# Kernel optimization log

Measured on AMD Instinct MI355X. Metric: run time of the kernel, lower is better.

## Reference

```python
import jax, jax.numpy as jnp
import numpy as np

B, M, D = 4, 2048, 1024


def setup_inputs() -> dict:
    key = jax.random.key(0)
    k1, k2, k3, k4 = jax.random.split(key, 4)
    x = jax.random.normal(k1, (B, M, D), dtype=jnp.float32)
    scale = 0.02
    wq = jax.random.normal(k2, (D, D), dtype=jnp.float32) * scale
    wk = jax.random.normal(k3, (D, D), dtype=jnp.float32) * scale
    wv = jax.random.normal(k4, (D, D), dtype=jnp.float32) * scale
    return {"x": x, "wq": wq, "wk": wk, "wv": wv}


def _rope_tables(m, d):
    # Faithful to source: phi = 10000 ** (-2*(i-1)/d)  (note the (i-1), incl. i=0)
    i = jnp.arange(d // 2, dtype=jnp.float32)
    phi = jnp.power(10000.0, -2.0 * (i - 1.0) / d)  # [d/2]
    pos = jnp.arange(m, dtype=jnp.float32)
    ang = pos[:, None] * phi[None, :]  # [m, d/2]
    return jnp.cos(ang), jnp.sin(ang)


def _apply_rope(t, cos, sin):
    # Original does t[pos] @ R[pos] (row-vector times rotation matrix):
    #   out_even =  t_even*cos + t_odd*sin
    #   out_odd  = -t_even*sin + t_odd*cos
    te = t[..., 0::2]  # [b, m, d/2]
    to = t[..., 1::2]
    oe = te * cos + to * sin
    oo = -te * sin + to * cos
    return jnp.stack([oe, oo], axis=-1).reshape(t.shape)


def reference(x, wq, wk, wv):
    b, m, d = x.shape
    q = x @ wq.T
    k = x @ wk.T
    v = x @ wv.T
    cos, sin = _rope_tables(m, d)
    qr = _apply_rope(q, cos, sin)
    kr = _apply_rope(k, cos, sin)
    # causal SDPA (dropout disabled for deterministic reference)
    scores = jnp.einsum('bqd,bkd->bqk', qr, kr) / jnp.sqrt(jnp.float32(d))
    causal = jnp.tril(jnp.ones((m, m), dtype=bool))
    scores = jnp.where(causal[None, :, :], scores, jnp.finfo(scores.dtype).min)
    attn = jax.nn.softmax(scores, axis=-1)
    return jnp.einsum('bqk,bkd->bqd', attn, v)
```

## Files before the change

### kernel.cpp

```cpp
#include <hip/hip_runtime.h>
#include <hip/hip_bf16.h>
#include <math.h>


typedef __bf16 bf16x8 __attribute__((ext_vector_type(8)));
typedef float  f32x4  __attribute__((ext_vector_type(4)));

__device__ __forceinline__ ushort f2bf(float f) {
    __hip_bfloat16 h = __float2bfloat16(f);
    return *reinterpret_cast<ushort*>(&h);
}

__device__ __forceinline__ void async_load16(const ushort* g, ushort* l) {
    __builtin_amdgcn_global_load_lds(
        (const __attribute__((address_space(1))) void*)g,
        (__attribute__((address_space(3))) void*)l, 16, 0, 0);
}

__global__ __launch_bounds__(256) void cvt_all_kernel(
    const float* __restrict__ x,  const float* __restrict__ wq,
    const float* __restrict__ wk, const float* __restrict__ wv,
    ushort* __restrict__ xb, ushort* __restrict__ wqb,
    ushort* __restrict__ wkb, ushort* __restrict__ wvb,
    float2* __restrict__ cs)
{
    const int t = blockIdx.y;
    if (t == 4) {
        const int idx = blockIdx.x * 256 + threadIdx.x;
        if (idx < 2048 * 512) {
            const int pos = idx >> 9, i = idx & 511;
            const float phi = powf(10000.0f, -2.0f * ((float)i - 1.0f) / 1024.0f);
            float s, c;
            sincosf((float)pos * phi, &s, &c);
            cs[idx] = make_float2(c, s);
        }
        return;
    }
    const float* in  = (t == 0) ? x  : (t == 1) ? wq  : (t == 2) ? wk  : wv;
    ushort*      out = (t == 0) ? xb : (t == 1) ? wqb : (t == 2) ? wkb : wvb;
    const int n4 = (t == 0) ? 2097152 : 262144;
    int i = blockIdx.x * blockDim.x + threadIdx.x;
    if (i < n4) {
        float4 f = ((const float4*)in)[i];
        ushort4 o;
        o.x = f2bf(f.x); o.y = f2bf(f.y); o.z = f2bf(f.z); o.w = f2bf(f.w);
        ((ushort4*)out)[i] = o;
    }
}

__device__ __forceinline__ void gemm128_core_sb(
    const ushort* __restrict__ A, const ushort* __restrict__ B,
    int lda, int ldb, int m0, int n0, int kIters,
    ushort* As, ushort* Bs, f32x4 acc[4][4])
{
    const int tid  = threadIdx.x;
    const int lane = tid & 63, wave = tid >> 6;
    const int wm = (wave >> 1) * 64, wn = (wave & 1) * 64;
    const int quad = lane >> 4, l16 = lane & 15;
    const int srow = lane >> 2, c = lane & 3;
    const int rr   = wave * 32 + srow;
    const int cc   = c ^ ((rr >> 1) & 3);
    const int scol = cc * 8;

    const ushort* ag0 = A + (size_t)(m0 + rr) * lda + scol;
    const ushort* bg0 = B + (size_t)(n0 + rr) * ldb + scol;
    const ushort* ag1 = ag0 + (size_t)16 * lda;
    const ushort* bg1 = bg0 + (size_t)16 * ldb;
    ushort* la0 = As + (wave * 32) * 32;
    ushort* la1 = la0 + 16 * 32;
    ushort* lb0 = Bs + (wave * 32) * 32;
    ushort* lb1 = lb0 + 16 * 32;

    for (int kt = 0; kt < kIters; ++kt) {
        const int k0 = kt * 32;
        async_load16(ag0 + k0, la0);
        async_load16(ag1 + k0, la1);
        async_load16(bg0 + k0, lb0);
        async_load16(bg1 + k0, lb1);
        __syncthreads();
        bf16x8 aF[4], bF[4];
#pragma unroll
        for (int i = 0; i < 4; ++i) {
            const int r = wm + i * 16 + l16;
            aF[i] = *(const bf16x8*)(As + r * 32 + ((quad ^ ((r >> 1) & 3)) * 8));
        }
#pragma unroll
        for (int j = 0; j < 4; ++j) {
            const int r = wn + j * 16 + l16;
            bF[j] = *(const bf16x8*)(Bs + r * 32 + ((quad ^ ((r >> 1) & 3)) * 8));
        }
#pragma unroll
        for (int i = 0; i < 4; ++i)
#pragma unroll
            for (int j = 0; j < 4; ++j)
                acc[i][j] = __builtin_amdgcn_mfma_f32_16x16x32_bf16(aF[i], bF[j], acc[i][j], 0, 0, 0);
        __syncthreads();
    }
}

__device__ __forceinline__ void gemm128_core_ring(
    const ushort* __restrict__ A, const ushort* __restrict__ B,
    int lda, int ldb, int m0, int n0, int kIters,
    ushort* L, f32x4 acc[4][4])
{
    const int tid  = threadIdx.x;
    const int lane = tid & 63, wave = tid >> 6;
    const int wm = (wave >> 1) * 64, wn = (wave & 1) * 64;
    const int quad = lane >> 4, l16 = lane & 15;
    const int srow = lane >> 2, c = lane & 3;
    const int rr   = wave * 32 + srow;
    const int cc   = c ^ ((rr >> 1) & 3);
    const int scol = cc * 8;

    const ushort* ag0 = A + (size_t)(m0 + rr) * lda + scol;
    const ushort* bg0 = B + (size_t)(n0 + rr) * ldb + scol;
    const ushort* ag1 = ag0 + (size_t)16 * lda;
    const ushort* bg1 = bg0 + (size_t)16 * ldb;
    const int lofs = (wave * 32) * 32;

#define RING_STAGE(KT, BUF) do {                                   \
        const int _k0 = (KT) * 32;                                 \
        ushort* _la = L + (BUF) * 4096 + lofs;                     \
        ushort* _lb = L + 12288 + (BUF) * 4096 + lofs;             \
        async_load16(ag0 + _k0, _la);                              \
        async_load16(ag1 + _k0, _la + 16 * 32);                    \
        async_load16(bg0 + _k0, _lb);                              \
        async_load16(bg1 + _k0, _lb + 16 * 32);                    \
    } while (0)

    RING_STAGE(0, 0);
    if (kIters > 1) RING_STAGE(1, 1);

    int buf = 0;
    for (int kt = 0; kt < kIters; ++kt) {
        if (kt + 1 < kIters) {
            asm volatile("s_waitcnt vmcnt(4)" ::: "memory");
        } else {
            asm volatile("s_waitcnt vmcnt(0)" ::: "memory");
        }
        __builtin_amdgcn_s_barrier();
        asm volatile("" ::: "memory");
        if (kt + 2 < kIters) {
            int nb = buf + 2; if (nb >= 3) nb -= 3;
            RING_STAGE(kt + 2, nb);
        }
        const ushort* as = L + buf * 4096;
        const ushort* bs = L + 12288 + buf * 4096;
        bf16x8 aF[4], bF[4];
#pragma unroll
        for (int i = 0; i < 4; ++i) {
            const int r = wm + i * 16 + l16;
            aF[i] = *(const bf16x8*)(as + r * 32 + ((quad ^ ((r >> 1) & 3)) * 8));
        }
#pragma unroll
        for (int j = 0; j < 4; ++j) {
            const int r = wn + j * 16 + l16;
            bF[j] = *(const bf16x8*)(bs + r * 32 + ((quad ^ ((r >> 1) & 3)) * 8));
        }
#pragma unroll
        for (int i = 0; i < 4; ++i)
#pragma unroll
            for (int j = 0; j < 4; ++j)
                acc[i][j] = __builtin_amdgcn_mfma_f32_16x16x32_bf16(aF[i], bF[j], acc[i][j], 0, 0, 0);
        buf += 1; if (buf == 3) buf = 0;
    }
#undef RING_STAGE
}

#define ACC_INIT4(acc) \
    _Pragma("unroll") for (int i = 0; i < 4; ++i) \
    _Pragma("unroll") for (int j = 0; j < 4; ++j) \
    _Pragma("unroll") for (int r = 0; r < 4; ++r) acc[i][j][r] = 0.0f;

__global__ __launch_bounds__(256) void qkv_rope_kernel(
    const ushort* __restrict__ xb, const ushort* __restrict__ wq,
    const ushort* __restrict__ wk, const ushort* __restrict__ wv,
    const float2* __restrict__ cs,
    ushort* __restrict__ Qr, ushort* __restrict__ Kr, ushort* __restrict__ VT)
{
    __shared__ __attribute__((aligned(16))) ushort As[128 * 32];
    __shared__ __attribute__((aligned(16))) ushort Bs[128 * 32];
    const int m0 = blockIdx.x * 128;
    const int n0 = blockIdx.y * 128;
    const int z  = blockIdx.z;
    const ushort* W = (z == 0) ? wq : (z == 1) ? wk : wv;

    f32x4 acc[4][4];
    ACC_INIT4(acc)
    gemm128_core_sb(xb, W, 1024, 1024, m0, n0, 32, As, Bs, acc);

    const int lane = threadIdx.x & 63, wave = threadIdx.x >> 6;
    const int wm = (wave >> 1) * 64, wn = (wave & 1) * 64;
    const int quad = lane >> 4, l16 = lane & 15;

    if (z < 2) {
        ushort* out = (z == 0) ? Qr : Kr;
#pragma unroll
        for (int j = 0; j < 4; ++j) {
            const int n = n0 + wn + j * 16 + l16;
            const int iidx = n >> 1;
            const bool odd = n & 1;
#pragma unroll
            for (int i = 0; i < 4; ++i) {
                const int mbase = m0 + wm + i * 16 + quad * 4;
                const int pos0  = mbase & 2047;
                const float2* csp = cs + (size_t)pos0 * 512 + iidx;
#pragma unroll
                for (int r = 0; r < 4; ++r) {
                    const float2 sc = csp[(size_t)r * 512];
                    float v = acc[i][j][r];
                    float p = __shfl_xor(v, 1);
                    float o = odd ? (v * sc.x - p * sc.y) : (v * sc.x + p * sc.y);
                    out[(size_t)(mbase + r) * 1024 + n] = f2bf(o);
                }
            }
        }
    } else {
#pragma unroll
        for (int i = 0; i < 4; ++i) {
            const int mbase = m0 + wm + i * 16 + quad * 4;
            const int b = mbase >> 11, pos0 = mbase & 2047;
#pragma unroll
            for (int j = 0; j < 4; ++j) {
                const int n = n0 + wn + j * 16 + l16;
                ushort4 o;
                o.x = f2bf(acc[i][j][0]); o.y = f2bf(acc[i][j][1]);
                o.z = f2bf(acc[i][j][2]); o.w = f2bf(acc[i][j][3]);
                *(ushort4*)(VT + ((size_t)b * 1024 + n) * 2048 + pos0) = o;
            }
        }
    }
}

__global__ __launch_bounds__(256) void scores_kernel(
    const ushort* __restrict__ Qr, const ushort* __restrict__ Kr,
    float* __restrict__ S)
{
    const int m0 = blockIdx.x * 128;
    const int n0 = blockIdx.y * 128;
    if (n0 > m0 + 127) return;
    const int b = blockIdx.z;
    __shared__ __attribute__((aligned(16))) ushort L[6 * 4096];
    const ushort* A = Qr + (size_t)b * 2048 * 1024;
    const ushort* B = Kr + (size_t)b * 2048 * 1024;
    float* Sb = S + (size_t)b * 2048 * 2048;

    f32x4 acc[4][4];
    ACC_INIT4(acc)
    gemm128_core_ring(A, B, 1024, 1024, m0, n0, 32, L, acc);

    const int lane = threadIdx.x & 63, wave = threadIdx.x >> 6;
    const int wm = (wave >> 1) * 64, wn = (wave & 1) * 64;
    const int quad = lane >> 4, l16 = lane & 15;
#pragma unroll
    for (int i = 0; i < 4; ++i)
#pragma unroll
        for (int j = 0; j < 4; ++j) {
            const int n = n0 + wn + j * 16 + l16;
#pragma unroll
            for (int r = 0; r < 4; ++r) {
                const int m = m0 + wm + i * 16 + quad * 4 + r;
                Sb[(size_t)m * 2048 + n] = acc[i][j][r] * 0.03125f;
            }
        }
}

__global__ __launch_bounds__(256) void softmax_kernel(
    const float* __restrict__ S, ushort* __restrict__ P)
{
    __shared__ float red[256];
    const int row = blockIdx.x, tid = threadIdx.x, b = blockIdx.y;
    const float* s = S + ((size_t)b * 2048 + row) * 2048;
    ushort*      p = P + ((size_t)b * 2048 + row) * 2048;
    const int nvalid = row + 1;
    const int wlimit = (row & ~127) + 128;
    const int j0 = tid * 8;

    float v[8] = {0.0f, 0.0f, 0.0f, 0.0f, 0.0f, 0.0f, 0.0f, 0.0f};
    if (j0 < nvalid) {
        float4 f0 = *(const float4*)(s + j0);
        v[0]=f0.x; v[1]=f0.y; v[2]=f0.z; v[3]=f0.w;
    }
    if (j0 + 4 < nvalid) {
        float4 f1 = *(const float4*)(s + j0 + 4);
        v[4]=f1.x; v[5]=f1.y; v[6]=f1.z; v[7]=f1.w;
    }

    float mx = -3.402823466e38f;
#pragma unroll
    for (int u = 0; u < 8; ++u) if (j0 + u < nvalid) mx = fmaxf(mx, v[u]);
    red[tid] = mx; __syncthreads();
    for (int off = 128; off > 0; off >>= 1) {
        if (tid < off) red[tid] = fmaxf(red[tid], red[tid + off]);
        __syncthreads();
    }
    mx = red[0]; __syncthreads();

    float sum = 0.0f;
#pragma unroll
    for (int u = 0; u < 8; ++u) {
        v[u] = (j0 + u < nvalid) ? __expf(v[u] - mx) : 0.0f;
        sum += v[u];
    }
    red[tid] = sum; __syncthreads();
    for (int off = 128; off > 0; off >>= 1) {
        if (tid < off) red[tid] += red[tid + off];
        __syncthreads();
    }
    const float inv = 1.0f / red[0];

    if (j0 < wlimit) {
        ushort o[8];
#pragma unroll
        for (int u = 0; u < 8; ++u) o[u] = f2bf(v[u] * inv);
        *(int4*)(p + j0) = *(const int4*)o;
    }
}

__global__ __launch_bounds__(256) void pv_kernel(
    const ushort* __restrict__ P, const ushort* __restrict__ VT,
    float* __restrict__ out)
{
    __shared__ __attribute__((aligned(16))) ushort L[6 * 4096];
    const int x  = blockIdx.x;
    const int mt = (x & 1) ? (15 - (x >> 1)) : (x >> 1);
    const int m0 = mt * 128;
    const int n0 = blockIdx.y * 128;
    const int b  = blockIdx.z;
    const ushort* A = P + (size_t)b * 2048 * 2048;
    const ushort* B = VT + (size_t)b * 1024 * 2048;
    const int kIters = (m0 + 128) / 32;

    f32x4 acc[4][4];
    ACC_INIT4(acc)
    gemm128_core_ring(A, B, 2048, 2048, m0, n0, kIters, L, acc);

    const int lane = threadIdx.x & 63, wave = threadIdx.x >> 6;
    const int wm = (wave >> 1) * 64, wn = (wave & 1) * 64;
    const int quad = lane >> 4, l16 = lane & 15;
#pragma unroll
    for (int i = 0; i < 4; ++i)
#pragma unroll
        for (int j = 0; j < 4; ++j) {
            const int n = n0 + wn + j * 16 + l16;
#pragma unroll
            for (int r = 0; r < 4; ++r) {
                const int m = m0 + wm + i * 16 + quad * 4 + r;
                out[((size_t)b * 2048 + m) * 1024 + n] = acc[i][j][r];
            }
        }
}

extern "C" void kernel_launch(void* const* d_in, const int* in_sizes, int n_in,
                              void* d_out, int out_size, void* d_ws, size_t ws_size,
                              hipStream_t stream) {
    const float* x  = (const float*)d_in[0];
    const float* wq = (const float*)d_in[1];
    const float* wk = (const float*)d_in[2];
    const float* wv = (const float*)d_in[3];

    const size_t MiB = 1024 * 1024;
    char* ws = (char*)d_ws;
    ushort* xb  = (ushort*)(ws);
    ushort* wqb = (ushort*)(ws +  16 * MiB);
    ushort* wkb = (ushort*)(ws +  18 * MiB);
    ushort* wvb = (ushort*)(ws +  20 * MiB);
    ushort* Qr  = (ushort*)(ws +  22 * MiB);
    ushort* Kr  = (ushort*)(ws +  38 * MiB);
    ushort* VT  = (ushort*)(ws +  54 * MiB);
    float*  S   = (float* )(ws +  70 * MiB);
    ushort* P   = (ushort*)(ws + 134 * MiB);
    float2* cs  = (float2*)(ws + 166 * MiB);
    float*  out = (float*)d_out;

    cvt_all_kernel <<<dim3(8192, 5),   256, 0, stream>>>(x, wq, wk, wv, xb, wqb, wkb, wvb, cs);
    qkv_rope_kernel<<<dim3(64, 8, 3),  256, 0, stream>>>(xb, wqb, wkb, wvb, cs, Qr, Kr, VT);
    scores_kernel  <<<dim3(16, 16, 4), 256, 0, stream>>>(Qr, Kr, S);
    softmax_kernel <<<dim3(2048, 4),   256, 0, stream>>>(S, P);
    pv_kernel      <<<dim3(16, 8, 4),  256, 0, stream>>>(P, VT, out);
}
```

Baseline: 271.6 us.

## Fuse softmax into scores epilogue and PV prologue via per-tile max/sum

Removes the standalone softmax kernel. The scores kernel now computes per-row max and exp-sum for each 128-column tile, and the PV kernel combines these tile stats, exponentiates the fp32 scores on the fly into bf16 shared-memory tiles, and rescales the output by the inverse row sum. This drops one launch and the write/read of the bf16 P matrix, but the PV kernel now reads fp32 scores (twice the bytes of P) and does exp work inside its main loop, with only double-buffered manual staging instead of the previous ring pipeline.

```diff
diff --git a/kernel.cpp b/kernel.cpp
--- a/kernel.cpp
+++ b/kernel.cpp
@@ -15,6 +15,19 @@
     __builtin_amdgcn_global_load_lds(
         (const __attribute__((address_space(1))) void*)g,
         (__attribute__((address_space(3))) void*)l, 16, 0, 0);
+}
+
+__device__ __forceinline__ void stage_a16(
+    ushort* dst, float4 lo, float4 hi, float m, int nv)
+{
+    float s[8] = {lo.x, lo.y, lo.z, lo.w, hi.x, hi.y, hi.z, hi.w};
+    ushort o[8];
+#pragma unroll
+    for (int u = 0; u < 8; ++u) {
+        const float e = (u < nv) ? __expf(s[u] - m) : 0.0f;
+        o[u] = f2bf(e);
+    }
+    *(int4*)dst = *(const int4*)o;
 }
 
 __global__ __launch_bounds__(256) void cvt_all_kernel(
@@ -234,13 +247,15 @@
 
 __global__ __launch_bounds__(256) void scores_kernel(
     const ushort* __restrict__ Qr, const ushort* __restrict__ Kr,
-    float* __restrict__ S)
+    float* __restrict__ S, float* __restrict__ Smax, float* __restrict__ Ssum)
 {
     const int m0 = blockIdx.x * 128;
     const int n0 = blockIdx.y * 128;
     if (n0 > m0 + 127) return;
     const int b = blockIdx.z;
     __shared__ __attribute__((aligned(16))) ushort L[6 * 4096];
+    __shared__ float scrM[128][2];
+    __shared__ float scrS[128][2];
     const ushort* A = Qr + (size_t)b * 2048 * 1024;
     const ushort* B = Kr + (size_t)b * 2048 * 1024;
     float* Sb = S + (size_t)b * 2048 * 2048;
@@ -263,81 +278,164 @@
                 Sb[(size_t)m * 2048 + n] = acc[i][j][r] * 0.03125f;
             }
         }
-}
-
-__global__ __launch_bounds__(256) void softmax_kernel(
-    const float* __restrict__ S, ushort* __restrict__ P)
-{
-    __shared__ float red[256];
-    const int row = blockIdx.x, tid = threadIdx.x, b = blockIdx.y;
-    const float* s = S + ((size_t)b * 2048 + row) * 2048;
-    ushort*      p = P + ((size_t)b * 2048 + row) * 2048;
-    const int nvalid = row + 1;
-    const int wlimit = (row & ~127) + 128;
-    const int j0 = tid * 8;
-
-    float v[8] = {0.0f, 0.0f, 0.0f, 0.0f, 0.0f, 0.0f, 0.0f, 0.0f};
-    if (j0 < nvalid) {
-        float4 f0 = *(const float4*)(s + j0);
-        v[0]=f0.x; v[1]=f0.y; v[2]=f0.z; v[3]=f0.w;
-    }
-    if (j0 + 4 < nvalid) {
-        float4 f1 = *(const float4*)(s + j0 + 4);
-        v[4]=f1.x; v[5]=f1.y; v[6]=f1.z; v[7]=f1.w;
-    }
-
-    float mx = -3.402823466e38f;
-#pragma unroll
-    for (int u = 0; u < 8; ++u) if (j0 + u < nvalid) mx = fmaxf(mx, v[u]);
-    red[tid] = mx; __syncthreads();
-    for (int off = 128; off > 0; off >>= 1) {
-        if (tid < off) red[tid] = fmaxf(red[tid], red[tid + off]);
-        __syncthreads();
-    }
-    mx = red[0]; __syncthreads();
-
-    float sum = 0.0f;
-#pragma unroll
-    for (int u = 0; u < 8; ++u) {
-        v[u] = (j0 + u < nvalid) ? __expf(v[u] - mx) : 0.0f;
-        sum += v[u];
-    }
-    red[tid] = sum; __syncthreads();
-    for (int off = 128; off > 0; off >>= 1) {
-        if (tid < off) red[tid] += red[tid + off];
-        __syncthreads();
-    }
-    const float inv = 1.0f / red[0];
-
-    if (j0 < wlimit) {
-        ushort o[8];
-#pragma unroll
-        for (int u = 0; u < 8; ++u) o[u] = f2bf(v[u] * inv);
-        *(int4*)(p + j0) = *(const int4*)o;
+
+    const int relq  = wm + quad * 4;
+    const int gcol0 = n0 + wn + l16;
+    float tm[4][4];
+#pragma unroll
+    for (int i = 0; i < 4; ++i)
+#pragma unroll
+        for (int r = 0; r < 4; ++r) {
+            const int grow = m0 + relq + i * 16 + r;
+            float mv = -3.402823466e38f;
+#pragma unroll
+            for (int j = 0; j < 4; ++j)
+                if (gcol0 + j * 16 <= grow) mv = fmaxf(mv, acc[i][j][r] * 0.03125f);
+#pragma unroll
+            for (int d = 1; d < 16; d <<= 1) mv = fmaxf(mv, __shfl_xor(mv, d));
+            if (l16 == 0) scrM[relq + i * 16 + r][wave & 1] = mv;
+        }
+    __syncthreads();
+#pragma unroll
+    for (int i = 0; i < 4; ++i)
+#pragma unroll
+        for (int r = 0; r < 4; ++r) {
+            const int rel = relq + i * 16 + r;
+            tm[i][r] = fmaxf(scrM[rel][0], scrM[rel][1]);
+        }
+#pragma unroll
+    for (int i = 0; i < 4; ++i)
+#pragma unroll
+        for (int r = 0; r < 4; ++r) {
+            const int grow = m0 + relq + i * 16 + r;
+            float ps = 0.0f;
+#pragma unroll
+            for (int j = 0; j < 4; ++j)
+                if (gcol0 + j * 16 <= grow)
+                    ps += __expf(acc[i][j][r] * 0.03125f - tm[i][r]);
+#pragma unroll
+            for (int d = 1; d < 16; d <<= 1) ps += __shfl_xor(ps, d);
+            if (l16 == 0) scrS[relq + i * 16 + r][wave & 1] = ps;
+        }
+    __syncthreads();
+    if ((wave & 1) == 0 && l16 == 0) {
+        const int nt = blockIdx.y;
+#pragma unroll
+        for (int i = 0; i < 4; ++i)
+#pragma unroll
+            for (int r = 0; r < 4; ++r) {
+                const int rel = relq + i * 16 + r;
+                const size_t sidx = ((size_t)b * 16 + nt) * 2048 + (m0 + rel);
+                Smax[sidx] = tm[i][r];
+                Ssum[sidx] = scrS[rel][0] + scrS[rel][1];
+            }
     }
 }
 
 __global__ __launch_bounds__(256) void pv_kernel(
-    const ushort* __restrict__ P, const ushort* __restrict__ VT,
+    const float* __restrict__ S, const ushort* __restrict__ VT,
+    const float* __restrict__ Smax, const float* __restrict__ Ssum,
     float* __restrict__ out)
 {
-    __shared__ __attribute__((aligned(16))) ushort L[6 * 4096];
+    __shared__ __attribute__((aligned(16))) ushort Abuf[2 * 4096];
+    __shared__ __attribute__((aligned(16))) ushort Bbuf[2 * 4096];
+    __shared__ float Mli[128][2];
     const int x  = blockIdx.x;
     const int mt = (x & 1) ? (15 - (x >> 1)) : (x >> 1);
     const int m0 = mt * 128;
     const int n0 = blockIdx.y * 128;
     const int b  = blockIdx.z;
-    const ushort* A = P + (size_t)b * 2048 * 2048;
-    const ushort* B = VT + (size_t)b * 1024 * 2048;
+    const float*  Sb = S + (size_t)b * 2048 * 2048;
+    const ushort* B  = VT + (size_t)b * 1024 * 2048;
     const int kIters = (m0 + 128) / 32;
+    const int tid = threadIdx.x;
+
+    if (tid < 128) {
+        const size_t sb0 = (size_t)b * 16 * 2048 + (m0 + tid);
+        float M = -3.402823466e38f;
+        for (int nt = 0; nt <= mt; ++nt)
+            M = fmaxf(M, Smax[sb0 + (size_t)nt * 2048]);
+        float Ls = 0.0f;
+        for (int nt = 0; nt <= mt; ++nt)
+            Ls += Ssum[sb0 + (size_t)nt * 2048] *
+                  __expf(Smax[sb0 + (size_t)nt * 2048] - M);
+        Mli[tid][0] = M;
+        Mli[tid][1] = 1.0f / Ls;
+    }
+    __syncthreads();
+
+    const int lane = tid & 63, wave = tid >> 6;
+    const int wm = (wave >> 1) * 64, wn = (wave & 1) * 64;
+    const int quad = lane >> 4, l16 = lane & 15;
+    const int srow = lane >> 2, c = lane & 3;
+    const int rr   = wave * 32 + srow;
+    const int cc   = c ^ ((rr >> 1) & 3);
+    const int scol = cc * 8;
+
+    const float*  sA0 = Sb + (size_t)(m0 + rr) * 2048 + scol;
+    const float*  sA1 = sA0 + (size_t)16 * 2048;
+    const ushort* bg0 = B + (size_t)(n0 + rr) * 2048 + scol;
+    const ushort* bg1 = bg0 + (size_t)16 * 2048;
+    const int ofs = wave * 1024 + lane * 8;
+    const float mr0 = Mli[rr][0];
+    const float mr1 = Mli[rr + 16][0];
+    const int vr0 = m0 + rr;
+    const int vr1 = m0 + rr + 16;
 
     f32x4 acc[4][4];
     ACC_INIT4(acc)
-    gemm128_core_ring(A, B, 2048, 2048, m0, n0, kIters, L, acc);
-
-    const int lane = threadIdx.x & 63, wave = threadIdx.x >> 6;
-    const int wm = (wave >> 1) * 64, wn = (wave & 1) * 64;
-    const int quad = lane >> 4, l16 = lane & 15;
+
+    {
+        float4 a0 = *(const float4*)(sA0);
+        float4 a1 = *(const float4*)(sA0 + 4);
+        float4 a2 = *(const float4*)(sA1);
+        float4 a3 = *(const float4*)(sA1 + 4);
+        stage_a16(Abuf + ofs,       a0, a1, mr0, vr0 - scol + 1);
+        stage_a16(Abuf + ofs + 512, a2, a3, mr1, vr1 - scol + 1);
+        async_load16(bg0, Bbuf + ofs);
+        async_load16(bg1, Bbuf + ofs + 512);
+    }
+    __syncthreads();
+
+    int cur = 0;
+    for (int kt = 0; kt < kIters; ++kt) {
+        float4 p0, p1, p2, p3;
+        const bool hn = (kt + 1 < kIters);
+        const int k1 = (kt + 1) * 32;
+        if (hn) {
+            p0 = *(const float4*)(sA0 + k1);
+            p1 = *(const float4*)(sA0 + k1 + 4);
+            p2 = *(const float4*)(sA1 + k1);
+            p3 = *(const float4*)(sA1 + k1 + 4);
+            async_load16(bg0 + k1, Bbuf + (cur ^ 1) * 4096 + ofs);
+            async_load16(bg1 + k1, Bbuf + (cur ^ 1) * 4096 + ofs + 512);
+        }
+        const ushort* as = Abuf + cur * 4096;
+        const ushort* bs = Bbuf + cur * 4096;
+        bf16x8 aF[4], bF[4];
+#pragma unroll
+        for (int i = 0; i < 4; ++i) {
+            const int r = wm + i * 16 + l16;
+            aF[i] = *(const bf16x8*)(as + r * 32 + ((quad ^ ((r >> 1) & 3)) * 8));
+        }
+#pragma unroll
+        for (int j = 0; j < 4; ++j) {
+            const int r = wn + j * 16 + l16;
+            bF[j] = *(const bf16x8*)(bs + r * 32 + ((quad ^ ((r >> 1) & 3)) * 8));
+        }
+#pragma unroll
+        for (int i = 0; i < 4; ++i)
+#pragma unroll
+            for (int j = 0; j < 4; ++j)
+                acc[i][j] = __builtin_amdgcn_mfma_f32_16x16x32_bf16(aF[i], bF[j], acc[i][j], 0, 0, 0);
+        if (hn) {
+            stage_a16(Abuf + (cur ^ 1) * 4096 + ofs,       p0, p1, mr0, vr0 - k1 - scol + 1);
+            stage_a16(Abuf + (cur ^ 1) * 4096 + ofs + 512, p2, p3, mr1, vr1 - k1 - scol + 1);
+        }
+        __syncthreads();
+        cur ^= 1;
+    }
+
 #pragma unroll
     for (int i = 0; i < 4; ++i)
 #pragma unroll
@@ -345,8 +443,9 @@
             const int n = n0 + wn + j * 16 + l16;
 #pragma unroll
             for (int r = 0; r < 4; ++r) {
-                const int m = m0 + wm + i * 16 + quad * 4 + r;
-                out[((size_t)b * 2048 + m) * 1024 + n] = acc[i][j][r];
+                const int rel = wm + i * 16 + quad * 4 + r;
+                const int m = m0 + rel;
+                out[((size_t)b * 2048 + m) * 1024 + n] = acc[i][j][r] * Mli[rel][1];
             }
         }
 }
@@ -369,13 +468,13 @@
     ushort* Kr  = (ushort*)(ws +  38 * MiB);
     ushort* VT  = (ushort*)(ws +  54 * MiB);
     float*  S   = (float* )(ws +  70 * MiB);
-    ushort* P   = (ushort*)(ws + 134 * MiB);
+    float*  Smax= (float* )(ws + 134 * MiB);
+    float*  Ssum= (float* )(ws + 135 * MiB);
     float2* cs  = (float2*)(ws + 166 * MiB);
     float*  out = (float*)d_out;
 
     cvt_all_kernel <<<dim3(8192, 5),   256, 0, stream>>>(x, wq, wk, wv, xb, wqb, wkb, wvb, cs);
     qkv_rope_kernel<<<dim3(64, 8, 3),  256, 0, stream>>>(xb, wqb, wkb, wvb, cs, Qr, Kr, VT);
-    scores_kernel  <<<dim3(16, 16, 4), 256, 0, stream>>>(Qr, Kr, S);
-    softmax_kernel <<<dim3(2048, 4),   256, 0, stream>>>(S, P);
-    pv_kernel      <<<dim3(16, 8, 4),  256, 0, stream>>>(P, VT, out);
-}
+    scores_kernel  <<<dim3(16, 16, 4), 256, 0, stream>>>(Qr, Kr, S, Smax, Ssum);
+    pv_kernel      <<<dim3(16, 8, 4),  256, 0, stream>>>(S, VT, Smax, Ssum, out);
+}
```

Result: slower. 311.6 us (+14.7%).
